# Kernel optimization log

Measured on AMD Instinct MI355X. Metric: run time of the kernel, lower is better.

## Reference

```python
import jax, jax.numpy as jnp
import numpy as np

B, N, C = 8, 4096, 768
H, M = 12, 64          # num_heads, num_landmarks
D = C // H             # head_dim = 64


def setup_inputs() -> dict:
    key = jax.random.key(0)
    k1, k2, k3, k4 = jax.random.split(key, 4)
    s = 0.02
    return {
        "x": jax.random.normal(k1, (B, N, C), dtype=jnp.float32),
        "w_qkv": jax.random.normal(k2, (3 * C, C), dtype=jnp.float32) * s,
        "w_proj": jax.random.normal(k3, (C, C), dtype=jnp.float32) * s,
        "b_proj": jax.random.normal(k4, (C,), dtype=jnp.float32) * s,
    }


def iterative_inv(mat, n_iter=6):
    # mat: [B, H, M, M]; Newton-Schulz cubic iteration for pseudo-inverse
    I = jnp.eye(mat.shape[-1], dtype=mat.dtype)
    K = mat
    # init: K^T / max_j(sum_i K_ij)  per (B,H)
    scale = jnp.max(jnp.sum(K, axis=-2), axis=-1)[:, :, None, None]
    V = jnp.swapaxes(K, -1, -2) / scale
    for _ in range(n_iter):
        KV = K @ V
        V = 0.25 * V @ (13.0 * I - KV @ (15.0 * I - KV @ (7.0 * I - KV)))
    return V


def reference(x, w_qkv, w_proj, b_proj):
    b, n, c = x.shape
    qkv = (x @ w_qkv.T).reshape(b, n, 3, H, D).transpose(2, 0, 3, 1, 4)  # [3,B,H,N,D]
    Q, K, V = qkv[0], qkv[1], qkv[2]
    Q = Q / (D ** 0.5)
    # landmark pooling (N % M == 0 path): segment means of length N//M
    Kl = K.reshape(b, H, M, n // M, D).mean(axis=-2)  # [B,H,M,D]
    Ql = Q.reshape(b, H, M, n // M, D).mean(axis=-2)  # [B,H,M,D]
    kernel1 = jax.nn.softmax(jnp.einsum('bhnd,bhmd->bhnm', Q, Kl), axis=-1)   # [B,H,N,M]
    kernel2 = jax.nn.softmax(jnp.einsum('bhmd,bhld->bhml', Ql, Kl), axis=-1)  # [B,H,M,M]
    kernel3 = jax.nn.softmax(jnp.einsum('bhmd,bhnd->bhmn', Ql, K), axis=-1)   # [B,H,M,N]
    SV = (kernel1 @ iterative_inv(kernel2)) @ (kernel3 @ V)  # [B,H,N,D]
    SV = SV.transpose(0, 2, 1, 3).reshape(b, n, c)
    out = SV @ w_proj.T + b_proj
    out = out + V.transpose(0, 2, 1, 3).reshape(b, n, c)
    return out
```

## Files before the change

kernel.cpp:

```cpp
#include <hip/hip_runtime.h>
#include <hip/hip_bf16.h>
#include <stdint.h>

typedef __bf16 bf16;
typedef __bf16 bf16x8 __attribute__((ext_vector_type(8)));
typedef __bf16 bf16x4 __attribute__((ext_vector_type(4)));
typedef float f32x4 __attribute__((ext_vector_type(4)));

#define B_ 8
#define N_ 4096
#define C_ 768
#define H_ 12
#define M_ 64
#define D_ 64
#define NT_ 32768
#define C3_ 2304

typedef __attribute__((address_space(3))) void lds_void_t;
typedef const __attribute__((address_space(1))) void gvoid_t;

__device__ __forceinline__ void gl_lds16(const void* gsrc, void* ldst) {
  __builtin_amdgcn_global_load_lds((gvoid_t*)(uintptr_t)gsrc,
                                   (lds_void_t*)(uintptr_t)ldst, 16, 0, 0);
}

__device__ __forceinline__ f32x4 mfma16(bf16x8 a, bf16x8 b, f32x4 c) {
  return __builtin_amdgcn_mfma_f32_16x16x32_bf16(a, b, c, 0, 0, 0);
}

#define VMW8 asm volatile("s_waitcnt vmcnt(8)" ::: "memory")
#define VMW4 asm volatile("s_waitcnt vmcnt(4)" ::: "memory")
#define VMW0 asm volatile("s_waitcnt vmcnt(0)" ::: "memory")
#define RAWBAR() { __builtin_amdgcn_sched_barrier(0); __builtin_amdgcn_s_barrier(); __builtin_amdgcn_sched_barrier(0); }

#define NX4   6291456
#define NW14  442368
#define NW24  147456
__global__ void k_cvt3(const float* __restrict__ x, bf16* __restrict__ xo,
                       const float* __restrict__ w1, bf16* __restrict__ w1o,
                       const float* __restrict__ w2, bf16* __restrict__ w2o) {
  const int stride = gridDim.x * blockDim.x;
  for (int i = blockIdx.x * blockDim.x + threadIdx.x; i < NX4 + NW14 + NW24; i += stride) {
    const float* src; bf16* dst; int idx;
    if (i < NX4)              { src = x;  dst = xo;  idx = i; }
    else if (i < NX4 + NW14)  { src = w1; dst = w1o; idx = i - NX4; }
    else                      { src = w2; dst = w2o; idx = i - NX4 - NW14; }
    f32x4 v = *(const f32x4*)(src + (size_t)idx * 4);
    bf16x4 o;
    o[0] = (bf16)v[0]; o[1] = (bf16)v[1]; o[2] = (bf16)v[2]; o[3] = (bf16)v[3];
    *(bf16x4*)(dst + (size_t)idx * 4) = o;
  }
}

__global__ __launch_bounds__(512, 2) void k_qkv(
    const bf16* __restrict__ xbf, const bf16* __restrict__ wbf,
    bf16* __restrict__ Qb, bf16* __restrict__ Kb, bf16* __restrict__ Vb,
    float* __restrict__ Qlf, float* __restrict__ Klf)
{
  __shared__ bf16 As[4][8192];
  __shared__ bf16 Bs[4][8192];
  const int t = threadIdx.x;
  const int wave = t >> 6, lane = t & 63;
  const int l15 = lane & 15, l16 = lane >> 4;

  const int bid = blockIdx.x;
  const int swz = (bid & 7) * 144 + (bid >> 3);
  const int bt = swz / 9, ct = swz % 9;
  const int row0 = bt * 256, ct0 = ct * 256;
  const int wr = wave >> 2, wc = wave & 3;

  const int srow = t >> 2;
  const int scol = (((t & 3) ^ ((t >> 3) & 3)) << 3);
  const bf16* gaBase = xbf + (size_t)(row0 + srow) * C_ + scol;
  const bf16* gbBase = wbf + (size_t)(ct0 + srow) * C_ + scol;

  const int aoff = (wr * 128 + l15) * 32 + ((l16 ^ ((l15 >> 1) & 3)) << 3);
  const int boff = (wc * 64 + l15) * 32 + ((l16 ^ ((l15 >> 1) & 3)) << 3);

  f32x4 acc[8][4] = {};
  bf16x8 afr0[4], afr1[4], bfr[2][4];

#define QSTAGE(kt3) {                                                            \
    const int sb_ = (kt3) & 3;                                                   \
    gl_lds16(gaBase + (kt3) * 32, &As[sb_][t * 8]);                              \
    gl_lds16(gbBase + (kt3) * 32, &Bs[sb_][t * 8]);                              \
    gl_lds16(gaBase + (size_t)128 * C_ + (kt3) * 32, &As[sb_][(t + 512) * 8]);   \
    gl_lds16(gbBase + (size_t)128 * C_ + (kt3) * 32, &Bs[sb_][(t + 512) * 8]); }

#define QKSTEP(kt, DO_STAGE, DO_NXT, VMW_, DO_BAR) {                             \
    if (DO_STAGE) QSTAGE((kt) + 3);                                             \
    { const bf16* asC = As[(kt) & 3];                                            \
      _Pragma("unroll")                                                          \
      for (int i = 0; i < 4; ++i)                                                \
        afr1[i] = *(const bf16x8*)&asC[aoff + (4 + i) * 512]; }                  \
    __builtin_amdgcn_s_setprio(1);                                               \
    _Pragma("unroll")                                                            \
    for (int i = 0; i < 4; ++i)                                                  \
      _Pragma("unroll")                                                          \
      for (int j = 0; j < 4; ++j)                                                \
        acc[i][j] = mfma16(afr0[i], bfr[(kt) & 1][j], acc[i][j]);                \
    __builtin_amdgcn_s_setprio(0);                                               \
    if (DO_NXT) {                                                                \
      const bf16* asN = As[((kt) + 1) & 3];                                      \
      const bf16* bsN = Bs[((kt) + 1) & 3];                                      \
      _Pragma("unroll")                                                          \
      for (int i = 0; i < 4; ++i)                                                \
        afr0[i] = *(const bf16x8*)&asN[aoff + i * 512];                          \
      _Pragma("unroll")                                                          \
      for (int j = 0; j < 4; ++j)                                                \
        bfr[((kt) + 1) & 1][j] = *(const bf16x8*)&bsN[boff + j * 512]; }         \
    __builtin_amdgcn_s_setprio(1);                                               \
    _Pragma("unroll")                                                            \
    for (int i = 0; i < 4; ++i)                                                  \
      _Pragma("unroll")                                                          \
      for (int j = 0; j < 4; ++j)                                                \
        acc[4 + i][j] = mfma16(afr1[i], bfr[(kt) & 1][j], acc[4 + i][j]);        \
    __builtin_amdgcn_s_setprio(0);                                               \
    VMW_;                                                                        \
    if (DO_BAR) RAWBAR(); }

  QSTAGE(0); QSTAGE(1); QSTAGE(2);
  VMW4;
  RAWBAR();
#pragma unroll
  for (int i = 0; i < 4; ++i) afr0[i] = *(const bf16x8*)&As[0][aoff + i * 512];
#pragma unroll
  for (int j = 0; j < 4; ++j) bfr[0][j] = *(const bf16x8*)&Bs[0][boff + j * 512];

  QKSTEP(0, 1, 1, VMW4, 1)  QKSTEP(1, 1, 1, VMW4, 1)  QKSTEP(2, 1, 1, VMW4, 1)
  QKSTEP(3, 1, 1, VMW4, 1)  QKSTEP(4, 1, 1, VMW4, 1)  QKSTEP(5, 1, 1, VMW4, 1)
  QKSTEP(6, 1, 1, VMW4, 1)  QKSTEP(7, 1, 1, VMW4, 1)  QKSTEP(8, 1, 1, VMW4, 1)
  QKSTEP(9, 1, 1, VMW4, 1)  QKSTEP(10, 1, 1, VMW4, 1) QKSTEP(11, 1, 1, VMW4, 1)
  QKSTEP(12, 1, 1, VMW4, 1) QKSTEP(13, 1, 1, VMW4, 1) QKSTEP(14, 1, 1, VMW4, 1)
  QKSTEP(15, 1, 1, VMW4, 1) QKSTEP(16, 1, 1, VMW4, 1) QKSTEP(17, 1, 1, VMW4, 1)
  QKSTEP(18, 1, 1, VMW4, 1) QKSTEP(19, 1, 1, VMW4, 1) QKSTEP(20, 1, 1, VMW4, 1)
  QKSTEP(21, 0, 1, VMW0, 1)
  QKSTEP(22, 0, 1, (void)0, 1)
  QKSTEP(23, 0, 0, (void)0, 0)

#undef QKSTEP
#undef QSTAGE

  const int colblock = ct0 + wc * 64;
  const int which = colblock / C_;
  const int h = (colblock % C_) / D_;
  const int b = row0 >> 12;
  const int n_base = (row0 & (N_ - 1)) + wr * 128;
  bf16* dst = (which == 0) ? Qb : (which == 1) ? Kb : Vb;
  const float scale = (which == 0) ? 0.125f : 1.0f;
  const size_t base = ((size_t)(b * H_ + h) * N_ + n_base) * D_;
#pragma unroll
  for (int i = 0; i < 8; ++i)
#pragma unroll
    for (int q = 0; q < 4; ++q) {
      const int rloc = i * 16 + l16 * 4 + q;
#pragma unroll
      for (int j = 0; j < 4; ++j) {
        const int d = j * 16 + l15;
        dst[base + (size_t)rloc * D_ + d] = (bf16)(acc[i][j][q] * scale);
      }
    }
  if (which < 2) {
    float* lmout = (which == 0) ? Qlf : Klf;
#pragma unroll
    for (int g = 0; g < 2; ++g) {
      const int m = (n_base >> 6) + g;
#pragma unroll
      for (int j = 0; j < 4; ++j) {
        float s = 0.f;
#pragma unroll
        for (int i = 4 * g; i < 4 * g + 4; ++i)
#pragma unroll
          for (int q = 0; q < 4; ++q) s += acc[i][j][q];
        s *= scale;
        s += __shfl_xor(s, 16);
        s += __shfl_xor(s, 32);
        if (l16 == 0)
          lmout[((size_t)(b * H_ + h) * M_ + m) * D_ + j * 16 + lane] = s * (1.0f / 64.0f);
      }
    }
  }
}

__global__ __launch_bounds__(512, 1) void k_inv(
    const float* __restrict__ Qlf, const float* __restrict__ Klf,
    float* __restrict__ pinv, bf16* __restrict__ Qlb, bf16* __restrict__ Klb)
{
  __shared__ float K2[4096];
  __shared__ float Vm[4096];
  __shared__ float KV[4096];
  __shared__ float T1[4096];
  __shared__ float U1[4096];
  __shared__ float tmp64[64];
  __shared__ float sscale;
  const int t = threadIdx.x;
  const int bh = blockIdx.x;
  const size_t off = (size_t)bh * 4096;
  for (int idx = t; idx < 4096; idx += 512) {
    const float q = Qlf[off + idx];
    T1[idx] = q;
    Qlb[off + idx] = (bf16)q;
  }
  for (int idx = t; idx < 4096; idx += 512) {
    const int r = idx >> 6, c = idx & 63;
    const float k = Klf[off + idx];
    U1[c * 64 + r] = k;
    Klb[off + idx] = (bf16)k;
  }
  __syncthreads();
  const int j0 = (t & 15) * 4;
  const int i0 = (t >> 4) * 2;

  auto MMstep = [&](const float* A, const float* Bm, float* O, float dg, float sg, float al) {
    float r2[2][4] = {};
    for (int k = 0; k < 64; ++k) {
      f32x4 bv = *(const f32x4*)&Bm[k * 64 + j0];
      const float a0 = A[(i0 + 0) * 64 + k];
      const float a1 = A[(i0 + 1) * 64 + k];
#pragma unroll
      for (int jj = 0; jj < 4; ++jj) { r2[0][jj] += a0 * bv[jj]; r2[1][jj] += a1 * bv[jj]; }
    }
#pragma unroll
    for (int ii = 0; ii < 2; ++ii)
#pragma unroll
      for (int jj = 0; jj < 4; ++jj)
        O[(i0 + ii) * 64 + j0 + jj] = al * (dg * A[(i0 + ii) * 64 + (j0 + jj)] + sg * r2[ii][jj]);
    __syncthreads();
  };

  {
    float r2[2][4] = {};
    for (int k = 0; k < 64; ++k) {
      f32x4 bv = *(const f32x4*)&U1[k * 64 + j0];
      const float a0 = T1[(i0 + 0) * 64 + k];
      const float a1 = T1[(i0 + 1) * 64 + k];
#pragma unroll
      for (int jj = 0; jj < 4; ++jj) { r2[0][jj] += a0 * bv[jj]; r2[1][jj] += a1 * bv[jj]; }
    }
#pragma unroll
    for (int ii = 0; ii < 2; ++ii)
#pragma unroll
      for (int jj = 0; jj < 4; ++jj)
        K2[(i0 + ii) * 64 + j0 + jj] = __expf(r2[ii][jj]);
  }
  __syncthreads();
  if (t < 64) {
    float s = 0.f;
    for (int k = 0; k < 64; ++k) s += K2[t * 64 + k];
    tmp64[t] = 1.0f / s;
  }
  __syncthreads();
  for (int idx = t; idx < 4096; idx += 512) K2[idx] *= tmp64[idx >> 6];
  __syncthreads();
  if (t < 64) {
    float s = 0.f;
    for (int i = 0; i < 64; ++i) s += K2[i * 64 + t];
    tmp64[t] = s;
  }
  __syncthreads();
  if (t == 0) {
    float mx = tmp64[0];
    for (int j2 = 1; j2 < 64; ++j2) mx = fmaxf(mx, tmp64[j2]);
    sscale = 1.0f / mx;
  }
  __syncthreads();
  for (int idx = t; idx < 4096; idx += 512) {
    const int r = idx >> 6, c = idx & 63;
    Vm[idx] = K2[c * 64 + r] * sscale;
  }
  __syncthreads();

  float* pV = Vm;
  float* pT = T1;
  for (int it = 0; it < 6; ++it) {
    MMstep(K2, pV, KV, 0.f, 1.f, 1.f);
    MMstep(KV, KV, pT, 7.f, -1.f, 1.f);
    MMstep(KV, pT, U1, 15.f, -1.f, 1.f);
    MMstep(pV, U1, pT, 13.f, -1.f, 0.25f);
    float* sw = pV; pV = pT; pT = sw;
  }
  for (int idx = t; idx < 4096; idx += 512) pinv[off + idx] = pV[idx];
}

__global__ __launch_bounds__(256, 2) void k_k3v(
    const bf16* __restrict__ Qlb, const bf16* __restrict__ Kb, const bf16* __restrict__ Vb,
    float* __restrict__ Zacc, float* __restrict__ rowsum_g)
{
  __shared__ bf16 Qls[64 * 64];
  __shared__ bf16 Ks[128 * 64];
  __shared__ bf16 Vs[128 * 64];
  __shared__ bf16 Ps[64 * 128];
  __shared__ float rs[64];
  const int t = threadIdx.x, wave = t >> 6, lane = t & 63;
  const int bh = blockIdx.x >> 3;
  const int chunk = blockIdx.x & 7;
  const size_t kvbase = (size_t)bh * N_ * D_ + (size_t)chunk * 512 * D_;
  {
    const bf16* g = Qlb + (size_t)bh * 4096;
    gl_lds16(g + t * 8, &Qls[t * 8]);
    gl_lds16(g + (t + 256) * 8, &Qls[(t + 256) * 8]);
  }
  if (t < 64) rs[t] = 0.f;
  f32x4 z[4] = {};
  for (int st = 0; st < 4; ++st) {
    const bf16* gk = Kb + kvbase + (size_t)st * 128 * D_;
    const bf16* gv = Vb + kvbase + (size_t)st * 128 * D_;
#pragma unroll
    for (int c = 0; c < 4; ++c) {
      gl_lds16(gk + (t + c * 256) * 8, &Ks[(t + c * 256) * 8]);
      gl_lds16(gv + (t + c * 256) * 8, &Vs[(t + c * 256) * 8]);
    }
    __syncthreads();
    f32x4 sacc[4][2] = {};
#pragma unroll
    for (int kk = 0; kk < 2; ++kk) {
      bf16x8 af[4], bk[2];
#pragma unroll
      for (int i = 0; i < 4; ++i)
        af[i] = *(const bf16x8*)&Qls[(i * 16 + (lane & 15)) * 64 + kk * 32 + 8 * (lane >> 4)];
#pragma unroll
      for (int j2 = 0; j2 < 2; ++j2)
        bk[j2] = *(const bf16x8*)&Ks[(wave * 32 + j2 * 16 + (lane & 15)) * 64 + kk * 32 + 8 * (lane >> 4)];
#pragma unroll
      for (int i = 0; i < 4; ++i)
#pragma unroll
        for (int j2 = 0; j2 < 2; ++j2)
          sacc[i][j2] = mfma16(af[i], bk[j2], sacc[i][j2]);
    }
#pragma unroll
    for (int i = 0; i < 4; ++i)
#pragma unroll
      for (int q = 0; q < 4; ++q) {
        const float e0 = __expf(sacc[i][0][q]);
        const float e1 = __expf(sacc[i][1][q]);
        const int m = i * 16 + (lane >> 4) * 4 + q;
        Ps[m * 128 + wave * 32 + (lane & 15)] = (bf16)e0;
        Ps[m * 128 + wave * 32 + 16 + (lane & 15)] = (bf16)e1;
        float p = e0 + e1;
        p += __shfl_xor(p, 1); p += __shfl_xor(p, 2);
        p += __shfl_xor(p, 4); p += __shfl_xor(p, 8);
        if ((lane & 15) == 0) atomicAdd(&rs[m], p);
      }
    __syncthreads();
#pragma unroll
    for (int kk = 0; kk < 4; ++kk) {
      const int kbase = kk * 32 + 8 * (lane >> 4);
      const int d = wave * 16 + (lane & 15);
      bf16x8 bv;
#pragma unroll
      for (int e = 0; e < 8; ++e) bv[e] = Vs[(kbase + e) * 64 + d];
#pragma unroll
      for (int i = 0; i < 4; ++i) {
        bf16x8 ap = *(const bf16x8*)&Ps[(i * 16 + (lane & 15)) * 128 + kbase];
        z[i] = mfma16(ap, bv, z[i]);
      }
    }
    __syncthreads();
  }
  const size_t zbase = (size_t)bh * 4096;
#pragma unroll
  for (int i = 0; i < 4; ++i)
#pragma unroll
    for (int q = 0; q < 4; ++q) {
      const int m = i * 16 + (lane >> 4) * 4 + q;
      const int d = wave * 16 + (lane & 15);
      atomicAdd(&Zacc[zbase + m * 64 + d], z[i][q]);
    }
  if (t < 64) atomicAdd(&rowsum_g[bh * 64 + t], rs[t]);
}

__global__ __launch_bounds__(256, 1) void k_comb(
    const float* __restrict__ pinv, const float* __restrict__ Zacc,
    const float* __restrict__ rowsum_g, bf16* __restrict__ Wtb)
{
  __shared__ float Pv[4096];
  __shared__ float Zn[4096];
  const int t = threadIdx.x, bh = blockIdx.x;
  const size_t off = (size_t)bh * 4096;
  for (int idx = t; idx < 4096; idx += 256) Pv[idx] = pinv[off + idx];
  for (int idx = t; idx < 4096; idx += 256)
    Zn[idx] = Zacc[off + idx] / rowsum_g[bh * 64 + (idx >> 6)];
  __syncthreads();
  const int j0 = (t & 15) * 4, i0 = (t >> 4) * 4;
  float r[4][4] = {{0.f}};
  for (int k = 0; k < 64; ++k) {
    f32x4 bv = *(const f32x4*)&Zn[k * 64 + j0];
    float a[4];
#pragma unroll
    for (int ii = 0; ii < 4; ++ii) a[ii] = Pv[(i0 + ii) * 64 + k];
#pragma unroll
    for (int ii = 0; ii < 4; ++ii)
#pragma unroll
      for (int jj = 0; jj < 4; ++jj) r[ii][jj] += a[ii] * bv[jj];
  }
#pragma unroll
  for (int ii = 0; ii < 4; ++ii)
#pragma unroll
    for (int jj = 0; jj < 4; ++jj)
      Wtb[off + (size_t)(j0 + jj) * 64 + (i0 + ii)] = (bf16)r[ii][jj];
}

__global__ __launch_bounds__(256, 2) void k_sv(
    const bf16* __restrict__ Qb, const bf16* __restrict__ Klb,
    const bf16* __restrict__ Wtb, bf16* __restrict__ SVb)
{
  __shared__ bf16 Qs[128 * 64];
  __shared__ bf16 Kls[64 * 64];
  __shared__ bf16 Wts[64 * 64];
  __shared__ bf16 Ps[128 * 64];
  const int t = threadIdx.x, wave = t >> 6, lane = t & 63;
  const int bh = blockIdx.x >> 5;
  const int nt = blockIdx.x & 31;
  const int b = bh / H_, h = bh % H_;
  {
    const bf16* gq = Qb + (size_t)bh * N_ * D_ + (size_t)nt * 128 * D_;
#pragma unroll
    for (int c = 0; c < 4; ++c) gl_lds16(gq + (t + c * 256) * 8, &Qs[(t + c * 256) * 8]);
    const bf16* gkl = Klb + (size_t)bh * 4096;
    gl_lds16(gkl + t * 8, &Kls[t * 8]);
    gl_lds16(gkl + (t + 256) * 8, &Kls[(t + 256) * 8]);
    const bf16* gw = Wtb + (size_t)bh * 4096;
    gl_lds16(gw + t * 8, &Wts[t * 8]);
    gl_lds16(gw + (t + 256) * 8, &Wts[(t + 256) * 8]);
  }
  __syncthreads();
  f32x4 sacc[2][4] = {};
#pragma unroll
  for (int kk = 0; kk < 2; ++kk) {
    bf16x8 af[2], bl[4];
#pragma unroll
    for (int r = 0; r < 2; ++r)
      af[r] = *(const bf16x8*)&Qs[(wave * 32 + r * 16 + (lane & 15)) * 64 + kk * 32 + 8 * (lane >> 4)];
#pragma unroll
    for (int j = 0; j < 4; ++j)
      bl[j] = *(const bf16x8*)&Kls[(j * 16 + (lane & 15)) * 64 + kk * 32 + 8 * (lane >> 4)];
#pragma unroll
    for (int r = 0; r < 2; ++r)
#pragma unroll
      for (int j = 0; j < 4; ++j)
        sacc[r][j] = mfma16(af[r], bl[j], sacc[r][j]);
  }
#pragma unroll
  for (int r = 0; r < 2; ++r)
#pragma unroll
    for (int q = 0; q < 4; ++q) {
      float e[4]; float s = 0.f;
#pragma unroll
      for (int j = 0; j < 4; ++j) { e[j] = __expf(sacc[r][j][q]); s += e[j]; }
      s += __shfl_xor(s, 1); s += __shfl_xor(s, 2);
      s += __shfl_xor(s, 4); s += __shfl_xor(s, 8);
      const float is = 1.0f / s;
      const int row = wave * 32 + r * 16 + (lane >> 4) * 4 + q;
#pragma unroll
      for (int j = 0; j < 4; ++j)
        Ps[row * 64 + j * 16 + (lane & 15)] = (bf16)(e[j] * is);
    }
  __syncthreads();
  f32x4 oacc[2][4] = {};
#pragma unroll
  for (int kk = 0; kk < 2; ++kk) {
    bf16x8 af[2], bw[4];
#pragma unroll
    for (int r = 0; r < 2; ++r)
      af[r] = *(const bf16x8*)&Ps[(wave * 32 + r * 16 + (lane & 15)) * 64 + kk * 32 + 8 * (lane >> 4)];
#pragma unroll
    for (int j = 0; j < 4; ++j)
      bw[j] = *(const bf16x8*)&Wts[(j * 16 + (lane & 15)) * 64 + kk * 32 + 8 * (lane >> 4)];
#pragma unroll
    for (int r = 0; r < 2; ++r)
#pragma unroll
      for (int j = 0; j < 4; ++j)
        oacc[r][j] = mfma16(af[r], bw[j], oacc[r][j]);
  }
  const size_t outbase = ((size_t)b * N_ + (size_t)nt * 128) * C_ + h * 64;
#pragma unroll
  for (int r = 0; r < 2; ++r)
#pragma unroll
    for (int q = 0; q < 4; ++q) {
      const int row = wave * 32 + r * 16 + (lane >> 4) * 4 + q;
#pragma unroll
      for (int j = 0; j < 4; ++j)
        SVb[outbase + (size_t)row * C_ + j * 16 + (lane & 15)] = (bf16)(oacc[r][j][q]);
    }
}

__global__ __launch_bounds__(256, 2) void k_proj(
    const bf16* __restrict__ SVb, const bf16* __restrict__ wpb,
    const float* __restrict__ bproj, const bf16* __restrict__ Vb,
    float* __restrict__ outp)
{
  __shared__ bf16 As[4][4096];
  __shared__ bf16 Bs[4][4096];
  const int t = threadIdx.x;
  const int wave = t >> 6, lane = t & 63;
  const int l15 = lane & 15, l16 = lane >> 4;
  const int bid = blockIdx.x;
  const int swz = (bid & 7) * 192 + (bid >> 3);
  const int bt = swz / 6, ct = swz % 6;
  const int row0 = bt * 128, col0 = ct * 128;
  const int wr = wave >> 1, wc = wave & 1;

  const int srow = t >> 2;
  const int scol = (((t & 3) ^ ((t >> 3) & 3)) << 3);
  const bf16* ga = SVb + (size_t)(row0 + srow) * C_ + scol;
  const bf16* gb = wpb + (size_t)(col0 + srow) * C_ + scol;

  const int aoff = (wr * 64 + l15) * 32 + ((l16 ^ ((l15 >> 1) & 3)) << 3);
  const int boff = (wc * 64 + l15) * 32 + ((l16 ^ ((l15 >> 1) & 3)) << 3);

  f32x4 acc[4][4] = {};
  bf16x8 afr[2][4], bfr[2][4];

#define PSTAGE(kt3) {                                                          \
    const int sb_ = (kt3) & 3;                                                 \
    gl_lds16(ga + (kt3) * 32, &As[sb_][t * 8]);                                \
    gl_lds16(gb + (kt3) * 32, &Bs[sb_][t * 8]);                                \
    gl_lds16(ga + (size_t)64 * C_ + (kt3) * 32, &As[sb_][(t + 256) * 8]);      \
    gl_lds16(gb + (size_t)64 * C_ + (kt3) * 32, &Bs[sb_][(t + 256) * 8]); }

#define PKSTEP(kt, DO_STAGE, DO_NXT, VMW_, DO_BAR) {                           \
    if (DO_STAGE) PSTAGE((kt) + 3);                                            \
    if (DO_NXT) {                                                              \
      const bf16* asN = As[((kt) + 1) & 3];                                    \
      const bf16* bsN = Bs[((kt) + 1) & 3];                                    \
      _Pragma("unroll")                                                        \
      for (int i = 0; i < 4; ++i)                                              \
        afr[((kt) + 1) & 1][i] = *(const bf16x8*)&asN[aoff + i * 512];         \
      _Pragma("unroll")                                                        \
      for (int j = 0; j < 4; ++j)                                              \
        bfr[((kt) + 1) & 1][j] = *(const bf16x8*)&bsN[boff + j * 512]; }       \
    __builtin_amdgcn_s_setprio(1);                                             \
    _Pragma("unroll")                                                          \
    for (int i = 0; i < 4; ++i)                                                \
      _Pragma("unroll")                                                        \
      for (int j = 0; j < 4; ++j)                                              \
        acc[i][j] = mfma16(afr[(kt) & 1][i], bfr[(kt) & 1][j], acc[i][j]);     \
    __builtin_amdgcn_s_setprio(0);                                             \
    VMW_;                                                                      \
    if (DO_BAR) RAWBAR(); }

  PSTAGE(0); PSTAGE(1); PSTAGE(2);
  VMW4;
  RAWBAR();
#pragma unroll
  for (int i = 0; i < 4; ++i) afr[0][i] = *(const bf16x8*)&As[0][aoff + i * 512];
#pragma unroll
  for (int j = 0; j < 4; ++j) bfr[0][j] = *(const bf16x8*)&Bs[0][boff + j * 512];

  PKSTEP(0, 1, 1, VMW4, 1)  PKSTEP(1, 1, 1, VMW4, 1)  PKSTEP(2, 1, 1, VMW4, 1)
  PKSTEP(3, 1, 1, VMW4, 1)  PKSTEP(4, 1, 1, VMW4, 1)  PKSTEP(5, 1, 1, VMW4, 1)
  PKSTEP(6, 1, 1, VMW4, 1)  PKSTEP(7, 1, 1, VMW4, 1)  PKSTEP(8, 1, 1, VMW4, 1)
  PKSTEP(9, 1, 1, VMW4, 1)  PKSTEP(10, 1, 1, VMW4, 1) PKSTEP(11, 1, 1, VMW4, 1)
  PKSTEP(12, 1, 1, VMW4, 1) PKSTEP(13, 1, 1, VMW4, 1) PKSTEP(14, 1, 1, VMW4, 1)
  PKSTEP(15, 1, 1, VMW4, 1) PKSTEP(16, 1, 1, VMW4, 1) PKSTEP(17, 1, 1, VMW4, 1)
  PKSTEP(18, 1, 1, VMW4, 1) PKSTEP(19, 1, 1, VMW4, 1) PKSTEP(20, 1, 1, VMW4, 1)
  PKSTEP(21, 0, 1, VMW0, 1)
  PKSTEP(22, 0, 1, (void)0, 1)
  PKSTEP(23, 0, 0, (void)0, 0)

#undef PKSTEP
#undef PSTAGE

#pragma unroll
  for (int i = 0; i < 4; ++i)
#pragma unroll
    for (int q = 0; q < 4; ++q) {
      const int row = row0 + wr * 64 + i * 16 + l16 * 4 + q;
      const int b = row >> 12, n = row & (N_ - 1);
#pragma unroll
      for (int j = 0; j < 4; ++j) {
        const int col = col0 + wc * 64 + j * 16 + l15;
        const int h = col >> 6, d = col & 63;
        const float v = acc[i][j][q] + bproj[col] +
                        (float)Vb[((size_t)(b * H_ + h) * N_ + n) * D_ + d];
        outp[(size_t)row * C_ + col] = v;
      }
    }
}

extern "C" void kernel_launch(void* const* d_in, const int* in_sizes, int n_in,
                              void* d_out, int out_size, void* d_ws, size_t ws_size,
                              hipStream_t stream) {
  const float* x = (const float*)d_in[0];
  const float* wqkv = (const float*)d_in[1];
  const float* wproj = (const float*)d_in[2];
  const float* bproj = (const float*)d_in[3];
  float* outp = (float*)d_out;
  char* ws = (char*)d_ws;

  size_t off = 0;
  auto take = [&](size_t bytes) { char* p = ws + off; off += bytes; return p; };
  bf16* xbf     = (bf16*)take(50331648);
  bf16* wqkvbf  = (bf16*)take(3538944);
  bf16* wprojbf = (bf16*)take(1179648);
  bf16* Qb      = (bf16*)take(50331648);
  bf16* Kb      = (bf16*)take(50331648);
  bf16* Vb      = (bf16*)take(50331648);
  float* Qlf    = (float*)take(1572864);
  float* Klf    = (float*)take(1572864);
  bf16* Qlb     = (bf16*)take(786432);
  bf16* Klb     = (bf16*)take(786432);
  float* pinvp  = (float*)take(1572864);
  float* Zacc   = (float*)take(1572864);
  float* rowsum = (float*)take(24576);
  bf16* Wtb     = (bf16*)take(786432);
  bf16* SVb     = xbf;

  hipMemsetAsync(Zacc, 0, 1572864 + 24576, stream);

  k_cvt3<<<2048, 256, 0, stream>>>(x, xbf, wqkv, wqkvbf, wproj, wprojbf);
  k_qkv<<<1152, 512, 0, stream>>>(xbf, wqkvbf, Qb, Kb, Vb, Qlf, Klf);
  k_inv<<<96, 512, 0, stream>>>(Qlf, Klf, pinvp, Qlb, Klb);
  k_k3v<<<768, 256, 0, stream>>>(Qlb, Kb, Vb, Zacc, rowsum);
  k_comb<<<96, 256, 0, stream>>>(pinvp, Zacc, rowsum, Wtb);
  k_sv<<<96 * 32, 256, 0, stream>>>(Qb, Klb, Wtb, SVb);
  k_proj<<<1536, 256, 0, stream>>>(SVb, wprojbf, bproj, Vb, outp);
}
```

Baseline: 378.1 us.

## Shrink QKV GEMM tile to 128x128 with simple double-buffered pipeline

Replaces the hand-scheduled 256x256, 4-stage, 512-thread QKV GEMM with a 128x128 tile, 256 threads and a plain two-buffer loop with a barrier each k-step. The aim is more blocks, lower LDS use and higher occupancy. It also raises launch bounds to 3 blocks per CU for k_sv and k_proj. In exchange, each block reuses its loaded data less, and the simpler pipeline loses the explicit prefetch depth and the interleaving of MFMA with LDS reads.

```diff
diff --git a/kernel.cpp b/kernel.cpp
--- a/kernel.cpp
+++ b/kernel.cpp
@@ -52,105 +52,70 @@
   }
 }
 
-__global__ __launch_bounds__(512, 2) void k_qkv(
+__global__ __launch_bounds__(256, 3) void k_qkv(
     const bf16* __restrict__ xbf, const bf16* __restrict__ wbf,
     bf16* __restrict__ Qb, bf16* __restrict__ Kb, bf16* __restrict__ Vb,
     float* __restrict__ Qlf, float* __restrict__ Klf)
 {
-  __shared__ bf16 As[4][8192];
-  __shared__ bf16 Bs[4][8192];
+  __shared__ bf16 As[2][128 * 32];
+  __shared__ bf16 Bs[2][128 * 32];
   const int t = threadIdx.x;
   const int wave = t >> 6, lane = t & 63;
   const int l15 = lane & 15, l16 = lane >> 4;
 
   const int bid = blockIdx.x;
-  const int swz = (bid & 7) * 144 + (bid >> 3);
-  const int bt = swz / 9, ct = swz % 9;
-  const int row0 = bt * 256, ct0 = ct * 256;
-  const int wr = wave >> 2, wc = wave & 3;
+  const int swz = (bid & 7) * 576 + (bid >> 3);
+  const int bt = swz / 18, ct = swz % 18;
+  const int row0 = bt * 128, col0 = ct * 128;
+  const int wr = wave >> 1, wc = wave & 1;
 
   const int srow = t >> 2;
   const int scol = (((t & 3) ^ ((t >> 3) & 3)) << 3);
-  const bf16* gaBase = xbf + (size_t)(row0 + srow) * C_ + scol;
-  const bf16* gbBase = wbf + (size_t)(ct0 + srow) * C_ + scol;
-
-  const int aoff = (wr * 128 + l15) * 32 + ((l16 ^ ((l15 >> 1) & 3)) << 3);
+  const bf16* ga = xbf + (size_t)(row0 + srow) * C_ + scol;
+  const bf16* gb = wbf + (size_t)(col0 + srow) * C_ + scol;
+
+  const int aoff = (wr * 64 + l15) * 32 + ((l16 ^ ((l15 >> 1) & 3)) << 3);
   const int boff = (wc * 64 + l15) * 32 + ((l16 ^ ((l15 >> 1) & 3)) << 3);
 
-  f32x4 acc[8][4] = {};
-  bf16x8 afr0[4], afr1[4], bfr[2][4];
-
-#define QSTAGE(kt3) {                                                            \
-    const int sb_ = (kt3) & 3;                                                   \
-    gl_lds16(gaBase + (kt3) * 32, &As[sb_][t * 8]);                              \
-    gl_lds16(gbBase + (kt3) * 32, &Bs[sb_][t * 8]);                              \
-    gl_lds16(gaBase + (size_t)128 * C_ + (kt3) * 32, &As[sb_][(t + 512) * 8]);   \
-    gl_lds16(gbBase + (size_t)128 * C_ + (kt3) * 32, &Bs[sb_][(t + 512) * 8]); }
-
-#define QKSTEP(kt, DO_STAGE, DO_NXT, VMW_, DO_BAR) {                             \
-    if (DO_STAGE) QSTAGE((kt) + 3);                                             \
-    { const bf16* asC = As[(kt) & 3];                                            \
-      _Pragma("unroll")                                                          \
-      for (int i = 0; i < 4; ++i)                                                \
-        afr1[i] = *(const bf16x8*)&asC[aoff + (4 + i) * 512]; }                  \
-    __builtin_amdgcn_s_setprio(1);                                               \
-    _Pragma("unroll")                                                            \
-    for (int i = 0; i < 4; ++i)                                                  \
-      _Pragma("unroll")                                                          \
-      for (int j = 0; j < 4; ++j)                                                \
-        acc[i][j] = mfma16(afr0[i], bfr[(kt) & 1][j], acc[i][j]);                \
-    __builtin_amdgcn_s_setprio(0);                                               \
-    if (DO_NXT) {                                                                \
-      const bf16* asN = As[((kt) + 1) & 3];                                      \
-      const bf16* bsN = Bs[((kt) + 1) & 3];                                      \
-      _Pragma("unroll")                                                          \
-      for (int i = 0; i < 4; ++i)                                                \
-        afr0[i] = *(const bf16x8*)&asN[aoff + i * 512];                          \
-      _Pragma("unroll")                                                          \
-      for (int j = 0; j < 4; ++j)                                                \
-        bfr[((kt) + 1) & 1][j] = *(const bf16x8*)&bsN[boff + j * 512]; }         \
-    __builtin_amdgcn_s_setprio(1);                                               \
-    _Pragma("unroll")                                                            \
-    for (int i = 0; i < 4; ++i)                                                  \
-      _Pragma("unroll")                                                          \
-      for (int j = 0; j < 4; ++j)                                                \
-        acc[4 + i][j] = mfma16(afr1[i], bfr[(kt) & 1][j], acc[4 + i][j]);        \
-    __builtin_amdgcn_s_setprio(0);                                               \
-    VMW_;                                                                        \
-    if (DO_BAR) RAWBAR(); }
-
-  QSTAGE(0); QSTAGE(1); QSTAGE(2);
-  VMW4;
-  RAWBAR();
-#pragma unroll
-  for (int i = 0; i < 4; ++i) afr0[i] = *(const bf16x8*)&As[0][aoff + i * 512];
-#pragma unroll
-  for (int j = 0; j < 4; ++j) bfr[0][j] = *(const bf16x8*)&Bs[0][boff + j * 512];
-
-  QKSTEP(0, 1, 1, VMW4, 1)  QKSTEP(1, 1, 1, VMW4, 1)  QKSTEP(2, 1, 1, VMW4, 1)
-  QKSTEP(3, 1, 1, VMW4, 1)  QKSTEP(4, 1, 1, VMW4, 1)  QKSTEP(5, 1, 1, VMW4, 1)
-  QKSTEP(6, 1, 1, VMW4, 1)  QKSTEP(7, 1, 1, VMW4, 1)  QKSTEP(8, 1, 1, VMW4, 1)
-  QKSTEP(9, 1, 1, VMW4, 1)  QKSTEP(10, 1, 1, VMW4, 1) QKSTEP(11, 1, 1, VMW4, 1)
-  QKSTEP(12, 1, 1, VMW4, 1) QKSTEP(13, 1, 1, VMW4, 1) QKSTEP(14, 1, 1, VMW4, 1)
-  QKSTEP(15, 1, 1, VMW4, 1) QKSTEP(16, 1, 1, VMW4, 1) QKSTEP(17, 1, 1, VMW4, 1)
-  QKSTEP(18, 1, 1, VMW4, 1) QKSTEP(19, 1, 1, VMW4, 1) QKSTEP(20, 1, 1, VMW4, 1)
-  QKSTEP(21, 0, 1, VMW0, 1)
-  QKSTEP(22, 0, 1, (void)0, 1)
-  QKSTEP(23, 0, 0, (void)0, 0)
-
-#undef QKSTEP
+  f32x4 acc[4][4] = {};
+
+#define QSTAGE(bi, k0) {                                                       \
+    gl_lds16(ga + (k0), &As[bi][t * 8]);                                       \
+    gl_lds16(gb + (k0), &Bs[bi][t * 8]);                                       \
+    gl_lds16(ga + (size_t)64 * C_ + (k0), &As[bi][(t + 256) * 8]);             \
+    gl_lds16(gb + (size_t)64 * C_ + (k0), &Bs[bi][(t + 256) * 8]); }
+
+  QSTAGE(0, 0);
+  __syncthreads();
+#pragma unroll 4
+  for (int ks = 0; ks < 24; ++ks) {
+    const int buf = ks & 1;
+    if (ks < 23) QSTAGE(buf ^ 1, (ks + 1) * 32);
+    bf16x8 af[4], bfr[4];
+#pragma unroll
+    for (int i = 0; i < 4; ++i) {
+      af[i]  = *(const bf16x8*)&As[buf][aoff + i * 512];
+      bfr[i] = *(const bf16x8*)&Bs[buf][boff + i * 512];
+    }
+#pragma unroll
+    for (int i = 0; i < 4; ++i)
+#pragma unroll
+      for (int j = 0; j < 4; ++j)
+        acc[i][j] = mfma16(af[i], bfr[j], acc[i][j]);
+    __syncthreads();
+  }
 #undef QSTAGE
 
-  const int colblock = ct0 + wc * 64;
+  const int colblock = col0 + wc * 64;
   const int which = colblock / C_;
   const int h = (colblock % C_) / D_;
   const int b = row0 >> 12;
-  const int n_base = (row0 & (N_ - 1)) + wr * 128;
+  const int n_base = (row0 & (N_ - 1)) + wr * 64;
   bf16* dst = (which == 0) ? Qb : (which == 1) ? Kb : Vb;
   const float scale = (which == 0) ? 0.125f : 1.0f;
   const size_t base = ((size_t)(b * H_ + h) * N_ + n_base) * D_;
 #pragma unroll
-  for (int i = 0; i < 8; ++i)
+  for (int i = 0; i < 4; ++i)
 #pragma unroll
     for (int q = 0; q < 4; ++q) {
       const int rloc = i * 16 + l16 * 4 + q;
@@ -162,22 +127,19 @@
     }
   if (which < 2) {
     float* lmout = (which == 0) ? Qlf : Klf;
-#pragma unroll
-    for (int g = 0; g < 2; ++g) {
-      const int m = (n_base >> 6) + g;
-#pragma unroll
-      for (int j = 0; j < 4; ++j) {
-        float s = 0.f;
-#pragma unroll
-        for (int i = 4 * g; i < 4 * g + 4; ++i)
-#pragma unroll
-          for (int q = 0; q < 4; ++q) s += acc[i][j][q];
-        s *= scale;
-        s += __shfl_xor(s, 16);
-        s += __shfl_xor(s, 32);
-        if (l16 == 0)
-          lmout[((size_t)(b * H_ + h) * M_ + m) * D_ + j * 16 + lane] = s * (1.0f / 64.0f);
-      }
+    const int m = n_base >> 6;
+#pragma unroll
+    for (int j = 0; j < 4; ++j) {
+      float s = 0.f;
+#pragma unroll
+      for (int i = 0; i < 4; ++i)
+#pragma unroll
+        for (int q = 0; q < 4; ++q) s += acc[i][j][q];
+      s *= scale;
+      s += __shfl_xor(s, 16);
+      s += __shfl_xor(s, 32);
+      if (l16 == 0)
+        lmout[((size_t)(b * H_ + h) * M_ + m) * D_ + j * 16 + lane] = s * (1.0f / 64.0f);
     }
   }
 }
@@ -400,7 +362,7 @@
       Wtb[off + (size_t)(j0 + jj) * 64 + (i0 + ii)] = (bf16)r[ii][jj];
 }
 
-__global__ __launch_bounds__(256, 2) void k_sv(
+__global__ __launch_bounds__(256, 3) void k_sv(
     const bf16* __restrict__ Qb, const bf16* __restrict__ Klb,
     const bf16* __restrict__ Wtb, bf16* __restrict__ SVb)
 {
@@ -484,7 +446,7 @@
     }
 }
 
-__global__ __launch_bounds__(256, 2) void k_proj(
+__global__ __launch_bounds__(256, 3) void k_proj(
     const bf16* __restrict__ SVb, const bf16* __restrict__ wpb,
     const float* __restrict__ bproj, const bf16* __restrict__ Vb,
     float* __restrict__ outp)
@@ -609,7 +571,7 @@
   hipMemsetAsync(Zacc, 0, 1572864 + 24576, stream);
 
   k_cvt3<<<2048, 256, 0, stream>>>(x, xbf, wqkv, wqkvbf, wproj, wprojbf);
-  k_qkv<<<1152, 512, 0, stream>>>(xbf, wqkvbf, Qb, Kb, Vb, Qlf, Klf);
+  k_qkv<<<4608, 256, 0, stream>>>(xbf, wqkvbf, Qb, Kb, Vb, Qlf, Klf);
   k_inv<<<96, 512, 0, stream>>>(Qlf, Klf, pinvp, Qlb, Klb);
   k_k3v<<<768, 256, 0, stream>>>(Qlb, Kb, Vb, Zacc, rowsum);
   k_comb<<<96, 256, 0, stream>>>(pinvp, Zacc, rowsum, Wtb);
```

Result: slower. 391.0 us (+3.4%).
